# Optimization experiments

Measured on AMD Instinct MI355X. Metric: run time of the kernel, lower is better.

## Reference

```python
import jax, jax.numpy as jnp
import numpy as np

NPOINT = 512
RADIUS = 0.1
NSAMPLE = 32
MLP_DIMS = [67, 64, 64, 128]  # 3 (rel xyz) + 64 feature channels -> ... -> 128


def setup_inputs() -> dict:
    key = jax.random.key(0)
    ks = jax.random.split(key, 8)
    N, C = 65536, 64
    xyz = jax.random.uniform(ks[0], (N, 3), dtype=jnp.float32)
    features = jax.random.normal(ks[1], (C, N), dtype=jnp.float32)
    inp = {"xyz": xyz, "features": features, "num_points": 8192}
    for i in range(3):
        cin, cout = MLP_DIMS[i], MLP_DIMS[i + 1]
        inp[f"W{i}"] = jax.random.normal(ks[2 + i], (cout, cin), dtype=jnp.float32) / np.sqrt(cin).astype(np.float32)
        inp[f"b{i}"] = jnp.zeros((cout,), jnp.float32)
    return inp


def _fps(pts, npoint):
    """Furthest point sampling for one example. pts: [n,3] -> [npoint] int32."""
    n = pts.shape[0]
    d0 = jnp.full((n,), 1e10, pts.dtype)

    def body(carry, _):
        dist, last = carry
        d = jnp.sum((pts - pts[last]) ** 2, axis=-1)
        dist = jnp.minimum(dist, d)
        nxt = jnp.argmax(dist).astype(jnp.int32)
        return (dist, nxt), nxt

    (_, _), rest = jax.lax.scan(body, (d0, jnp.int32(0)), None, length=npoint - 1)
    return jnp.concatenate([jnp.zeros((1,), jnp.int32), rest])


def _ball_query(centers, pts, radius, nsample):
    """centers: [m,3], pts: [n,3] -> [m,nsample] int32 (first nsample in-ball ids,
    padded with the first in-ball id, matching pointnet2 ball_query semantics)."""
    m = centers.shape[0]
    n = pts.shape[0]
    d2 = jnp.sum((centers[:, None, :] - pts[None, :, :]) ** 2, axis=-1)  # [m, n]
    mask = d2 < radius * radius
    pos = jnp.cumsum(mask.astype(jnp.int32), axis=-1)  # rank of each in-ball point
    first = jnp.argmax(mask, axis=-1).astype(jnp.int32)  # first in-ball idx (0 if none)
    default = jnp.broadcast_to(first[:, None], (m, nsample))
    # extra dump column at slot==nsample for out-of-ball / overflow entries
    init = jnp.concatenate([default, jnp.zeros((m, 1), jnp.int32)], axis=1)
    slot = jnp.where(mask & (pos <= nsample), pos - 1, nsample)  # [m, n]
    rows = jnp.broadcast_to(jnp.arange(m)[:, None], (m, n))
    cols = jnp.broadcast_to(jnp.arange(n, dtype=jnp.int32)[None, :], (m, n))
    idx = init.at[rows, slot].set(cols)
    return idx[:, :nsample]


def reference(xyz, features, num_points, W0, b0, W1, b1, W2, b2):
    N = xyz.shape[0]
    B = N // num_points
    C = features.shape[0]
    xyz_b = xyz.reshape(B, num_points, 3)                      # [B, n, 3]
    feat_b = features.reshape(C, B, num_points).transpose(1, 0, 2)  # [B, C, n]

    # FPS per example
    new_idx = jax.vmap(lambda p: _fps(p, NPOINT))(xyz_b)        # [B, npoint]
    new_xyz = jnp.take_along_axis(xyz_b, new_idx[..., None], axis=1)  # [B, npoint, 3]

    # ball query + grouping (QueryAndGroup, use_xyz=True)
    sample_ids = jax.vmap(lambda c, p: _ball_query(c, p, RADIUS, NSAMPLE))(new_xyz, xyz_b)  # [B, npoint, nsample]
    grouped_xyz = jax.vmap(lambda p, i: p[i])(xyz_b, sample_ids)      # [B, npoint, nsample, 3]
    grouped_xyz = grouped_xyz - new_xyz[:, :, None, :]                # relative coords
    grouped_feat = jax.vmap(lambda f, i: f[:, i])(feat_b, sample_ids)  # [B, C, npoint, nsample]
    g = jnp.concatenate([grouped_xyz.transpose(0, 3, 1, 2), grouped_feat], axis=1)  # [B, 3+C, npoint, nsample]

    # shared 1x1 conv MLP + ReLU, then max over the nsample dim
    h = g
    for W, b in ((W0, b0), (W1, b1), (W2, b2)):
        h = jax.nn.relu(jnp.einsum('oc,bcps->bops', W, h) + b[None, :, None, None])
    new_features = h.max(axis=-1)  # [B, 128, npoint]

    return new_xyz, new_idx, new_features, sample_ids
```

## Files before the change

### kernel.cpp

```cpp
#include <hip/hip_runtime.h>
#include <cstdint>
#include <cstddef>

#define NPOINT 512
#define NSAMPLE 32
#define NPB 8192

__device__ __forceinline__ unsigned short f2bf(float f) {
  unsigned int u = __float_as_uint(f);
  unsigned int r = u + 0x7FFFu + ((u >> 16) & 1u);
  return (unsigned short)(r >> 16);
}

__global__ __launch_bounds__(512) void k_fps(const float* __restrict__ xyz,
                                             float* __restrict__ out_xyz,
                                             float* __restrict__ out_idx) {
  const int b = blockIdx.x;
  const int t = threadIdx.x;
  const float* xb = xyz + (size_t)b * NPB * 3;

  float px[16], py[16], pz[16], dist[16];
  {
    const float4* gp = reinterpret_cast<const float4*>(xb + (size_t)t * 48);
    float comp[48];
#pragma unroll
    for (int v = 0; v < 12; ++v) {
      float4 r = gp[v];
      comp[v * 4 + 0] = r.x;
      comp[v * 4 + 1] = r.y;
      comp[v * 4 + 2] = r.z;
      comp[v * 4 + 3] = r.w;
    }
#pragma unroll
    for (int j = 0; j < 16; ++j) {
      px[j] = comp[3 * j + 0];
      py[j] = comp[3 * j + 1];
      pz[j] = comp[3 * j + 2];
      dist[j] = 1e10f;
    }
  }

  __shared__ __align__(16) float sD[2][8];
  __shared__ int sI[2][8];
  __shared__ float sX[2][8], sY[2][8], sZ[2][8];

  const int wid = t >> 6;
  const int lane = t & 63;

  float qx = xb[0], qy = xb[1], qz = xb[2];
  if (t == 0) {
    out_idx[b * NPOINT + 0] = 0.0f;
    size_t o = (size_t)(b * NPOINT) * 3;
    out_xyz[o + 0] = qx; out_xyz[o + 1] = qy; out_xyz[o + 2] = qz;
  }

  for (int it = 1; it < NPOINT; ++it) {
    float best = -1.0f;
    int bi = 0;
#pragma unroll
    for (int j = 0; j < 16; ++j) {
      float dx = __fsub_rn(px[j], qx);
      float dy = __fsub_rn(py[j], qy);
      float dz = __fsub_rn(pz[j], qz);
      float d2 = __fadd_rn(__fadd_rn(__fmul_rn(dx, dx), __fmul_rn(dy, dy)), __fmul_rn(dz, dz));
      float nd = fminf(dist[j], d2);
      dist[j] = nd;
      if (nd > best) { best = nd; bi = j; }
    }
    float wmax = best;
#pragma unroll
    for (int off = 32; off >= 1; off >>= 1) wmax = fmaxf(wmax, __shfl_xor(wmax, off));
    const unsigned long long m = __ballot(best == wmax);
    const int p = it & 1;
    if (lane == (int)(__ffsll((unsigned long long)m) - 1)) {
      sD[p][wid] = wmax;
      sI[p][wid] = t * 16 + bi;
      float sx_, sy_, sz_;
      switch (bi) {
        case 0:  sx_ = px[0];  sy_ = py[0];  sz_ = pz[0];  break;
        case 1:  sx_ = px[1];  sy_ = py[1];  sz_ = pz[1];  break;
        case 2:  sx_ = px[2];  sy_ = py[2];  sz_ = pz[2];  break;
        case 3:  sx_ = px[3];  sy_ = py[3];  sz_ = pz[3];  break;
        case 4:  sx_ = px[4];  sy_ = py[4];  sz_ = pz[4];  break;
        case 5:  sx_ = px[5];  sy_ = py[5];  sz_ = pz[5];  break;
        case 6:  sx_ = px[6];  sy_ = py[6];  sz_ = pz[6];  break;
        case 7:  sx_ = px[7];  sy_ = py[7];  sz_ = pz[7];  break;
        case 8:  sx_ = px[8];  sy_ = py[8];  sz_ = pz[8];  break;
        case 9:  sx_ = px[9];  sy_ = py[9];  sz_ = pz[9];  break;
        case 10: sx_ = px[10]; sy_ = py[10]; sz_ = pz[10]; break;
        case 11: sx_ = px[11]; sy_ = py[11]; sz_ = pz[11]; break;
        case 12: sx_ = px[12]; sy_ = py[12]; sz_ = pz[12]; break;
        case 13: sx_ = px[13]; sy_ = py[13]; sz_ = pz[13]; break;
        case 14: sx_ = px[14]; sy_ = py[14]; sz_ = pz[14]; break;
        default: sx_ = px[15]; sy_ = py[15]; sz_ = pz[15]; break;
      }
      sX[p][wid] = sx_; sY[p][wid] = sy_; sZ[p][wid] = sz_;
    }
    __syncthreads();
    float bd = sD[p][0];
    int bw = 0;
#pragma unroll
    for (int w = 1; w < 8; ++w) {
      float d = sD[p][w];
      if (d > bd) { bd = d; bw = w; }
    }
    const int gbi = sI[p][bw];
    qx = sX[p][bw]; qy = sY[p][bw]; qz = sZ[p][bw];
    if (t == 0) {
      out_idx[b * NPOINT + it] = (float)gbi;
      size_t o = (size_t)(b * NPOINT + it) * 3;
      out_xyz[o + 0] = qx; out_xyz[o + 1] = qy; out_xyz[o + 2] = qz;
    }
  }
}

__global__ __launch_bounds__(256) void k_transpose(const float* __restrict__ in,
                                                   unsigned short* __restrict__ out,
                                                   int Ntot) {
  __shared__ __align__(16) unsigned short tile[64][65];
  const int t = threadIdx.x;
  const int n0 = blockIdx.x * 64;
#pragma unroll
  for (int i = 0; i < 16; ++i) {
    int c = i * 4 + (t >> 6);
    int n = t & 63;
    tile[c][n] = f2bf(in[(size_t)c * Ntot + n0 + n]);
  }
  __syncthreads();
#pragma unroll
  for (int i = 0; i < 16; ++i) {
    int n = i * 4 + (t >> 6);
    int c = t & 63;
    out[(size_t)(n0 + n) * 64 + c] = tile[c][n];
  }
}

__global__ __launch_bounds__(512) void k_ball(const float* __restrict__ xyz,
                                              const float* __restrict__ fps_idx_f,
                                              float* __restrict__ sids_f) {
  __shared__ int slots[8 * NSAMPLE];
  const int b = blockIdx.x >> 6;
  const int cbase = (blockIdx.x & 63) * 8;
  const int t = threadIdx.x;
  const float* xb = xyz + (size_t)b * NPB * 3;

  const int w = t >> 6, lane = t & 63;
  const int c_local = cbase + w;
  const int ci = (int)fps_idx_f[b * NPOINT + c_local];
  const float cx = xb[ci * 3 + 0];
  const float cy = xb[ci * 3 + 1];
  const float cz = xb[ci * 3 + 2];
  const float R2 = 0.01f;
  const unsigned long long below = (1ull << lane) - 1ull;

  int cnt = 0;
#pragma unroll 4
  for (int r = 0; r < 64; ++r) {
    const int p0 = r * 128 + lane;
    const int p1 = p0 + 64;
    float ax = xb[p0 * 3 + 0], ay = xb[p0 * 3 + 1], az = xb[p0 * 3 + 2];
    float bx = xb[p1 * 3 + 0], by = xb[p1 * 3 + 1], bz = xb[p1 * 3 + 2];
    float dxa = __fsub_rn(ax, cx), dya = __fsub_rn(ay, cy), dza = __fsub_rn(az, cz);
    float dxb = __fsub_rn(bx, cx), dyb = __fsub_rn(by, cy), dzb = __fsub_rn(bz, cz);
    float d2a = __fadd_rn(__fadd_rn(__fmul_rn(dxa, dxa), __fmul_rn(dya, dya)), __fmul_rn(dza, dza));
    float d2b = __fadd_rn(__fadd_rn(__fmul_rn(dxb, dxb), __fmul_rn(dyb, dyb)), __fmul_rn(dzb, dzb));
    const bool i0 = d2a < R2;
    const bool i1 = d2b < R2;
    const unsigned long long m0 = __ballot(i0);
    if (i0) {
      int pos = cnt + (int)__popcll(m0 & below);
      if (pos < NSAMPLE) slots[w * NSAMPLE + pos] = p0;
    }
    cnt += (int)__popcll(m0);
    const unsigned long long m1 = __ballot(i1);
    if (i1) {
      int pos = cnt + (int)__popcll(m1 & below);
      if (pos < NSAMPLE) slots[w * NSAMPLE + pos] = p1;
    }
    cnt += (int)__popcll(m1);
  }
  if (lane < NSAMPLE) {
    const int first = (cnt > 0) ? slots[w * NSAMPLE] : 0;
    const int v = (lane < cnt) ? slots[w * NSAMPLE + lane] : first;
    sids_f[((size_t)(b * NPOINT + c_local)) * NSAMPLE + lane] = (float)v;
  }
}

__global__ __launch_bounds__(256) void k_mlp(const float* __restrict__ xyz,
                                             const float* __restrict__ feat,
                                             const unsigned short* __restrict__ feat_t,
                                             const float* __restrict__ fps_idx_f,
                                             const float* __restrict__ sids_f,
                                             const float* __restrict__ w0g,
                                             const float* __restrict__ b0g,
                                             const float* __restrict__ w1g,
                                             const float* __restrict__ b1g,
                                             const float* __restrict__ w2g,
                                             const float* __restrict__ b2g,
                                             float* __restrict__ out_feat,
                                             int Ntot, int useT) {
  __shared__ __align__(16) float W0s[64 * 68];
  __shared__ __align__(16) unsigned short W1s[64 * 64];
  __shared__ __align__(16) float W2s[128 * 64];
  __shared__ float b0s[64], b1s[64], b2s[128];
  const int t = threadIdx.x;
  for (int i = t; i < 64 * 68; i += 256) {
    int r = i / 68, c = i - r * 68;
    W0s[i] = (c < 67) ? w0g[r * 67 + c] : 0.0f;
  }
  for (int i = t; i < 64 * 64; i += 256) W1s[i] = f2bf(w1g[i]);
  for (int i = t; i < 128 * 64; i += 256) W2s[i] = w2g[i];
  if (t < 64) b0s[t] = b0g[t];
  if (t < 64) b1s[t] = b1g[t];
  if (t < 128) b2s[t] = b2g[t];
  __syncthreads();

  const int b = blockIdx.x >> 6;
  const int c_local = (blockIdx.x & 63) * 8 + (t >> 5);
  const int s = t & 31;
  const int ci = (int)fps_idx_f[b * NPOINT + c_local];
  const float cx = xyz[((size_t)b * NPB + ci) * 3 + 0];
  const float cy = xyz[((size_t)b * NPB + ci) * 3 + 1];
  const float cz = xyz[((size_t)b * NPB + ci) * 3 + 2];
  const int id = (int)sids_f[((size_t)(b * NPOINT + c_local)) * NSAMPLE + s];

  float g[68];
  {
    const size_t pb = ((size_t)b * NPB + id) * 3;
    g[0] = __fsub_rn(xyz[pb + 0], cx);
    g[1] = __fsub_rn(xyz[pb + 1], cy);
    g[2] = __fsub_rn(xyz[pb + 2], cz);
    if (useT) {
      const uint4* fp = reinterpret_cast<const uint4*>(feat_t + ((size_t)b * NPB + id) * 64);
#pragma unroll
      for (int v = 0; v < 8; ++v) {
        uint4 r = fp[v];
        unsigned int vs[4] = {r.x, r.y, r.z, r.w};
#pragma unroll
        for (int q = 0; q < 4; ++q) {
          g[3 + v * 8 + q * 2 + 0] = __uint_as_float(vs[q] << 16);
          g[3 + v * 8 + q * 2 + 1] = __uint_as_float(vs[q] & 0xFFFF0000u);
        }
      }
    } else {
      const float* col = feat + (size_t)(b * NPB + id);
#pragma unroll 8
      for (int c = 0; c < 64; ++c) g[3 + c] = col[(size_t)c * Ntot];
    }
    g[67] = 0.0f;
  }

  float h1[64];
#pragma unroll
  for (int o = 0; o < 64; ++o) {
    float acc = b0s[o];
    const float4* wp = reinterpret_cast<const float4*>(&W0s[o * 68]);
#pragma unroll
    for (int c4 = 0; c4 < 17; ++c4) {
      float4 wv = wp[c4];
      acc += wv.x * g[c4 * 4 + 0];
      acc += wv.y * g[c4 * 4 + 1];
      acc += wv.z * g[c4 * 4 + 2];
      acc += wv.w * g[c4 * 4 + 3];
    }
    h1[o] = fmaxf(acc, 0.0f);
  }
  float h2[64];
#pragma unroll
  for (int o = 0; o < 64; ++o) {
    float acc = b1s[o];
    const uint2* wp = reinterpret_cast<const uint2*>(&W1s[o * 64]);
#pragma unroll
    for (int c4 = 0; c4 < 16; ++c4) {
      uint2 u = wp[c4];
      acc += __uint_as_float(u.x << 16) * h1[c4 * 4 + 0];
      acc += __uint_as_float(u.x & 0xFFFF0000u) * h1[c4 * 4 + 1];
      acc += __uint_as_float(u.y << 16) * h1[c4 * 4 + 2];
      acc += __uint_as_float(u.y & 0xFFFF0000u) * h1[c4 * 4 + 3];
    }
    h2[o] = fmaxf(acc, 0.0f);
  }
#pragma unroll 1
  for (int o = 0; o < 128; ++o) {
    float acc = b2s[o];
    const float4* wp = reinterpret_cast<const float4*>(&W2s[o * 64]);
#pragma unroll
    for (int c4 = 0; c4 < 16; ++c4) {
      float4 wv = wp[c4];
      acc += wv.x * h2[c4 * 4 + 0];
      acc += wv.y * h2[c4 * 4 + 1];
      acc += wv.z * h2[c4 * 4 + 2];
      acc += wv.w * h2[c4 * 4 + 3];
    }
    float v = fmaxf(acc, 0.0f);
#pragma unroll
    for (int off = 16; off >= 1; off >>= 1) v = fmaxf(v, __shfl_xor(v, off));
    if (s == 0) out_feat[((size_t)b * 128 + o) * NPOINT + c_local] = v;
  }
}

extern "C" void kernel_launch(void* const* d_in, const int* in_sizes, int n_in,
                              void* d_out, int out_size, void* d_ws, size_t ws_size,
                              hipStream_t stream) {
  (void)n_in; (void)out_size;
  const float* xyz = (const float*)d_in[0];
  const float* feat = (const float*)d_in[1];
  const float* w0 = (const float*)d_in[3];
  const float* b0 = (const float*)d_in[4];
  const float* w1 = (const float*)d_in[5];
  const float* b1 = (const float*)d_in[6];
  const float* w2 = (const float*)d_in[7];
  const float* b2 = (const float*)d_in[8];

  const int Ntot = in_sizes[0] / 3;
  const int B = Ntot / NPB;

  float* out = (float*)d_out;
  float* o_xyz = out;
  float* o_idx = o_xyz + (size_t)B * NPOINT * 3;
  float* o_feat = o_idx + (size_t)B * NPOINT;
  float* o_sids = o_feat + (size_t)B * 128 * NPOINT;

  const size_t ft_bytes = (size_t)Ntot * 64 * 2;
  const int useT = (ws_size >= ft_bytes) ? 1 : 0;
  unsigned short* ft_ws = (unsigned short*)d_ws;

  if (useT) {
    k_transpose<<<dim3(Ntot / 64), dim3(256), 0, stream>>>(feat, ft_ws, Ntot);
  }
  k_fps<<<dim3(B), dim3(512), 0, stream>>>(xyz, o_xyz, o_idx);
  k_ball<<<dim3(B * 64), dim3(512), 0, stream>>>(xyz, o_idx, o_sids);
  k_mlp<<<dim3(B * 64), dim3(256), 0, stream>>>(xyz, feat, ft_ws, o_idx, o_sids,
                                                w0, b0, w1, b1, w2, b2, o_feat,
                                                Ntot, useT);
}
```

Before: 875.7 us.

## Read MLP weights from global memory and streamline FPS argmax

The MLP kernel stops staging its weights in LDS and reads them directly from global memory with uniform addresses, so the compiler can use scalar loads and the per-block staging and barrier go away. It also drops the bf16 rounding of W1. The FPS loop now computes the per-thread max with a tree of fmax operations and finds the argmax index only in the winning lane. Both kernels gain a minimum-occupancy launch bound, which may cause register spills given the large per-thread arrays.

```diff
diff --git a/kernel.cpp b/kernel.cpp
--- a/kernel.cpp
+++ b/kernel.cpp
@@ -12,9 +12,9 @@
   return (unsigned short)(r >> 16);
 }
 
-__global__ __launch_bounds__(512) void k_fps(const float* __restrict__ xyz,
-                                             float* __restrict__ out_xyz,
-                                             float* __restrict__ out_idx) {
+__global__ __launch_bounds__(512, 2) void k_fps(const float* __restrict__ xyz,
+                                                float* __restrict__ out_xyz,
+                                                float* __restrict__ out_idx) {
   const int b = blockIdx.x;
   const int t = threadIdx.x;
   const float* xb = xyz + (size_t)b * NPB * 3;
@@ -55,24 +55,31 @@
   }
 
   for (int it = 1; it < NPOINT; ++it) {
-    float best = -1.0f;
-    int bi = 0;
 #pragma unroll
     for (int j = 0; j < 16; ++j) {
       float dx = __fsub_rn(px[j], qx);
       float dy = __fsub_rn(py[j], qy);
       float dz = __fsub_rn(pz[j], qz);
       float d2 = __fadd_rn(__fadd_rn(__fmul_rn(dx, dx), __fmul_rn(dy, dy)), __fmul_rn(dz, dz));
-      float nd = fminf(dist[j], d2);
-      dist[j] = nd;
-      if (nd > best) { best = nd; bi = j; }
-    }
+      dist[j] = fminf(dist[j], d2);
+    }
+    float m01 = fmaxf(dist[0], dist[1]),   m23 = fmaxf(dist[2], dist[3]);
+    float m45 = fmaxf(dist[4], dist[5]),   m67 = fmaxf(dist[6], dist[7]);
+    float m89 = fmaxf(dist[8], dist[9]),   mab = fmaxf(dist[10], dist[11]);
+    float mcd = fmaxf(dist[12], dist[13]), mef = fmaxf(dist[14], dist[15]);
+    float q0 = fmaxf(fmaxf(m01, m23), fmaxf(m45, m67));
+    float q1 = fmaxf(fmaxf(m89, mab), fmaxf(mcd, mef));
+    float best = fmaxf(q0, q1);
     float wmax = best;
 #pragma unroll
     for (int off = 32; off >= 1; off >>= 1) wmax = fmaxf(wmax, __shfl_xor(wmax, off));
     const unsigned long long m = __ballot(best == wmax);
     const int p = it & 1;
     if (lane == (int)(__ffsll((unsigned long long)m) - 1)) {
+      int bi = 15;
+#pragma unroll
+      for (int j = 15; j >= 0; --j)
+        if (dist[j] == wmax) bi = j;
       sD[p][wid] = wmax;
       sI[p][wid] = t * 16 + bi;
       float sx_, sy_, sz_;
@@ -186,35 +193,20 @@
   }
 }
 
-__global__ __launch_bounds__(256) void k_mlp(const float* __restrict__ xyz,
-                                             const float* __restrict__ feat,
-                                             const unsigned short* __restrict__ feat_t,
-                                             const float* __restrict__ fps_idx_f,
-                                             const float* __restrict__ sids_f,
-                                             const float* __restrict__ w0g,
-                                             const float* __restrict__ b0g,
-                                             const float* __restrict__ w1g,
-                                             const float* __restrict__ b1g,
-                                             const float* __restrict__ w2g,
-                                             const float* __restrict__ b2g,
-                                             float* __restrict__ out_feat,
-                                             int Ntot, int useT) {
-  __shared__ __align__(16) float W0s[64 * 68];
-  __shared__ __align__(16) unsigned short W1s[64 * 64];
-  __shared__ __align__(16) float W2s[128 * 64];
-  __shared__ float b0s[64], b1s[64], b2s[128];
+__global__ __launch_bounds__(256, 2) void k_mlp(const float* __restrict__ xyz,
+                                                const float* __restrict__ feat,
+                                                const unsigned short* __restrict__ feat_t,
+                                                const float* __restrict__ fps_idx_f,
+                                                const float* __restrict__ sids_f,
+                                                const float* __restrict__ w0g,
+                                                const float* __restrict__ b0g,
+                                                const float* __restrict__ w1g,
+                                                const float* __restrict__ b1g,
+                                                const float* __restrict__ w2g,
+                                                const float* __restrict__ b2g,
+                                                float* __restrict__ out_feat,
+                                                int Ntot, int useT) {
   const int t = threadIdx.x;
-  for (int i = t; i < 64 * 68; i += 256) {
-    int r = i / 68, c = i - r * 68;
-    W0s[i] = (c < 67) ? w0g[r * 67 + c] : 0.0f;
-  }
-  for (int i = t; i < 64 * 64; i += 256) W1s[i] = f2bf(w1g[i]);
-  for (int i = t; i < 128 * 64; i += 256) W2s[i] = w2g[i];
-  if (t < 64) b0s[t] = b0g[t];
-  if (t < 64) b1s[t] = b1g[t];
-  if (t < 128) b2s[t] = b2g[t];
-  __syncthreads();
-
   const int b = blockIdx.x >> 6;
   const int c_local = (blockIdx.x & 63) * 8 + (t >> 5);
   const int s = t & 31;
@@ -224,7 +216,7 @@
   const float cz = xyz[((size_t)b * NPB + ci) * 3 + 2];
   const int id = (int)sids_f[((size_t)(b * NPOINT + c_local)) * NSAMPLE + s];
 
-  float g[68];
+  float g[67];
   {
     const size_t pb = ((size_t)b * NPB + id) * 3;
     g[0] = __fsub_rn(xyz[pb + 0], cx);
@@ -247,51 +239,32 @@
 #pragma unroll 8
       for (int c = 0; c < 64; ++c) g[3 + c] = col[(size_t)c * Ntot];
     }
-    g[67] = 0.0f;
   }
 
   float h1[64];
 #pragma unroll
   for (int o = 0; o < 64; ++o) {
-    float acc = b0s[o];
-    const float4* wp = reinterpret_cast<const float4*>(&W0s[o * 68]);
-#pragma unroll
-    for (int c4 = 0; c4 < 17; ++c4) {
-      float4 wv = wp[c4];
-      acc += wv.x * g[c4 * 4 + 0];
-      acc += wv.y * g[c4 * 4 + 1];
-      acc += wv.z * g[c4 * 4 + 2];
-      acc += wv.w * g[c4 * 4 + 3];
-    }
+    float acc = b0g[o];
+    const float* wr = w0g + o * 67;
+#pragma unroll
+    for (int c = 0; c < 67; ++c) acc += wr[c] * g[c];
     h1[o] = fmaxf(acc, 0.0f);
   }
   float h2[64];
 #pragma unroll
   for (int o = 0; o < 64; ++o) {
-    float acc = b1s[o];
-    const uint2* wp = reinterpret_cast<const uint2*>(&W1s[o * 64]);
-#pragma unroll
-    for (int c4 = 0; c4 < 16; ++c4) {
-      uint2 u = wp[c4];
-      acc += __uint_as_float(u.x << 16) * h1[c4 * 4 + 0];
-      acc += __uint_as_float(u.x & 0xFFFF0000u) * h1[c4 * 4 + 1];
-      acc += __uint_as_float(u.y << 16) * h1[c4 * 4 + 2];
-      acc += __uint_as_float(u.y & 0xFFFF0000u) * h1[c4 * 4 + 3];
-    }
+    float acc = b1g[o];
+    const float* wr = w1g + o * 64;
+#pragma unroll
+    for (int c = 0; c < 64; ++c) acc += wr[c] * h1[c];
     h2[o] = fmaxf(acc, 0.0f);
   }
 #pragma unroll 1
   for (int o = 0; o < 128; ++o) {
-    float acc = b2s[o];
-    const float4* wp = reinterpret_cast<const float4*>(&W2s[o * 64]);
-#pragma unroll
-    for (int c4 = 0; c4 < 16; ++c4) {
-      float4 wv = wp[c4];
-      acc += wv.x * h2[c4 * 4 + 0];
-      acc += wv.y * h2[c4 * 4 + 1];
-      acc += wv.z * h2[c4 * 4 + 2];
-      acc += wv.w * h2[c4 * 4 + 3];
-    }
+    float acc = b2g[o];
+    const float* wr = w2g + o * 64;
+#pragma unroll
+    for (int c = 0; c < 64; ++c) acc += wr[c] * h2[c];
     float v = fmaxf(acc, 0.0f);
 #pragma unroll
     for (int off = 16; off >= 1; off >>= 1) v = fmaxf(v, __shfl_xor(v, off));
```

New measurement: 961.5 us. 9.8% more time.
